# Optimization experiments

Hardware: AMD Instinct MI355X
Metric: run time of the kernel (lower is better)

## Reference

```python
import jax, jax.numpy as jnp
import numpy as np

B, L, Q, C, D = 256, 200, 20000, 500, 256
S = L - 1  # 199 recurrent steps, bounded by time_embed (200) / state banks (199)


def setup_inputs() -> dict:
    key = jax.random.key(0)
    ks = iter(jax.random.split(key, 48))
    nk = lambda: next(ks)

    def lin(fi, fo):
        w = jax.random.normal(nk(), (fo, fi), jnp.float32) * 0.02
        b = jnp.zeros((fo,), jnp.float32)
        return w, b

    inp = {}
    inp["question_seq"] = jax.random.randint(nk(), (B, L), 0, Q, dtype=jnp.int32)
    inp["concept_seq"] = jax.random.randint(nk(), (B, L), 0, C, dtype=jnp.int32)
    inp["correctness_seq"] = jax.random.randint(nk(), (B, L), 0, 2, dtype=jnp.int32)
    # parameters (torch.rand -> uniform[0,1))
    inp["pro_embed"] = jax.random.uniform(nk(), (Q, D), jnp.float32)
    inp["skill_embed"] = jax.random.uniform(nk(), (C, D), jnp.float32)
    inp["ans_embed"] = jax.random.uniform(nk(), (2, D), jnp.float32)
    inp["time_embed"] = jax.random.uniform(nk(), (200, D), jnp.float32)
    inp["ls_state"] = jax.random.uniform(nk(), (1, D), jnp.float32)
    inp["pro_state0"] = jax.random.uniform(nk(), (S, D), jnp.float32)
    inp["skill_state0"] = jax.random.uniform(nk(), (S, D), jnp.float32)
    inp["akt_pro_diff"] = jax.random.uniform(nk(), (Q, 1), jnp.float32)
    inp["akt_pro_change"] = jax.random.uniform(nk(), (C, D), jnp.float32)
    inp["Wpf"], inp["bpf"] = lin(2 * D, D)
    inp["Wps"], inp["bps"] = lin(2 * D, D)
    inp["Wsf"], inp["bsf"] = lin(2 * D, D)
    inp["Wss"], inp["bss"] = lin(2 * D, D)
    inp["Waf"], inp["baf"] = lin(2 * D, D)
    inp["Was"], inp["bas"] = lin(2 * D, D)
    inp["Wo1"], inp["bo1"] = lin(4 * D, D)
    inp["Wo2"], inp["bo2"] = lin(D, 1)
    return inp


def reference(question_seq, concept_seq, correctness_seq, pro_embed, skill_embed,
              ans_embed, time_embed, ls_state, pro_state0, skill_state0,
              akt_pro_diff, akt_pro_change, Wpf, bpf, Wps, bps, Wsf, bsf,
              Wss, bss, Waf, baf, Was, bas, Wo1, bo1, Wo2, bo2):
    nq = question_seq[:, 1:]   # [B,S] next problem ids
    nc = concept_seq[:, 1:]    # [B,S] next skill ids
    na = correctness_seq[:, 1:]
    # fused question embedding (Rasch-style): q + c + diff(q)*change(c)
    npe = pro_embed[nq] + skill_embed[nc] + akt_pro_diff[nq] * akt_pro_change[nc]  # [B,S,D]
    nx = npe + ans_embed[na]   # interaction embedding
    atge = time_embed[1]       # all_time_gap == 1 for every (b,t)
    bidx = jnp.arange(B)

    def step(carry, xs):
        lpt, lct, ps, ss, ast = carry  # last-time tables, time-indexed state banks, global state
        t, pe, x, ip, ic = xs
        lp_t = lpt[bidx, ip]           # [B] last time this problem was seen
        lp_s = ps[bidx, lp_t]          # [B,D] gather from problem state bank
        lc_t = lct[bidx, ic]
        lc_s = ss[bidx, lc_t]
        tge = time_embed[t - lp_t]
        ctge = time_embed[t - lc_t]
        # forget gates (dropout p=0 -> identity)
        lp_s = lp_s * jax.nn.sigmoid(jnp.concatenate([lp_s, tge], -1) @ Wpf.T + bpf)
        lc_s = lc_s * jax.nn.sigmoid(jnp.concatenate([lc_s, ctge], -1) @ Wsf.T + bsf)
        la_s = ast * jax.nn.sigmoid(
            jnp.concatenate([ast, jnp.broadcast_to(atge, ast.shape)], -1) @ Waf.T + baf)
        final = jnp.concatenate([la_s, lp_s, lc_s, pe], -1)  # [B,4D]
        P = jax.nn.sigmoid(jax.nn.relu(final @ Wo1.T + bo1) @ Wo2.T + bo2)[:, 0]
        # state updates
        a_new = la_s + jnp.tanh(jnp.concatenate([la_s, x], -1) @ Was.T + bas)
        p_new = lp_s + jnp.tanh(jnp.concatenate([lp_s, x], -1) @ Wps.T + bps)
        c_new = lc_s + jnp.tanh(jnp.concatenate([lc_s, x], -1) @ Wss.T + bss)
        lpt = lpt.at[bidx, ip].set(t)
        lct = lct.at[bidx, ic].set(t)
        ps = ps.at[:, t].set(p_new)   # scatter into time slot t
        ss = ss.at[:, t].set(c_new)
        return (lpt, lct, ps, ss, a_new), P

    init = (jnp.zeros((B, Q), jnp.int32),
            jnp.zeros((B, C), jnp.int32),
            jnp.broadcast_to(pro_state0[None], (B, S, D)) + 0.0,
            jnp.broadcast_to(skill_state0[None], (B, S, D)) + 0.0,
            jnp.broadcast_to(ls_state, (B, D)) + 0.0)
    ts = jnp.arange(S, dtype=jnp.int32)
    xs = (ts, jnp.swapaxes(npe, 0, 1), jnp.swapaxes(nx, 0, 1), nq.T, nc.T)
    _, Ps = jax.lax.scan(step, init, xs)  # Ps: [S,B]
    return Ps.T  # [B,S]
```

## Files before the change

kernel.cpp:

```cpp
#include <hip/hip_runtime.h>
#include <cstdint>
#include <cstddef>

#define B_ 256
#define L_ 200
#define S_ 199
#define D_ 256
#define Q_ 20000
#define C_ 500

#define OFF_TEPF 0u
#define OFF_TESF 204800u
#define OFF_CAF  409600u
#define OFF_PPF  410624u
#define OFF_PSF  541696u
#define OFF_PAF  672768u
#define OFF_PAS  803840u
#define OFF_PPS  1065984u
#define OFF_PSS  1328128u
#define OFF_PO1  1590272u
#define OFF_PS   2114560u
#define OFF_SS   54281216u

__device__ __forceinline__ unsigned bf16_rne(float f) {
  unsigned u = __float_as_uint(f);
  return (u + 0x7fffu + ((u >> 16) & 1u)) >> 16;
}

__global__ void te_kernel(const float* __restrict__ te,
                          const float* __restrict__ Wpf, const float* __restrict__ bpf,
                          const float* __restrict__ Wsf, const float* __restrict__ bsf,
                          float* __restrict__ TEpf, float* __restrict__ TEsf) {
  int idx = blockIdx.x * 256 + threadIdx.x;
  int tau = idx >> 8, d = idx & 255;
  const float* ter = te + (tau << 8);
  const float* wp = Wpf + d * 512 + 256;
  const float* ws = Wsf + d * 512 + 256;
  float ap = 0.f, as = 0.f;
  for (int k = 0; k < 256; ++k) {
    float x = ter[k];
    ap = fmaf(x, wp[k], ap);
    as = fmaf(x, ws[k], as);
  }
  TEpf[idx] = ap + bpf[d];
  TEsf[idx] = as + bsf[d];
}

__global__ void caf_kernel(const float* __restrict__ te, const float* __restrict__ Waf,
                           const float* __restrict__ baf, float* __restrict__ CAF) {
  int d = threadIdx.x;
  const float* ter = te + 256;
  const float* wa = Waf + d * 512 + 256;
  float a = 0.f;
  for (int k = 0; k < 256; ++k) a = fmaf(ter[k], wa[k], a);
  CAF[d] = a + baf[d];
}

__global__ void pack_kernel(const float* __restrict__ W, uint2* __restrict__ out, int fi) {
  int k4 = blockIdx.x, d = threadIdx.x;
  const float* r = W + d * fi + (k4 << 2);
  unsigned p0 = bf16_rne(r[0]) | (bf16_rne(r[1]) << 16);
  unsigned p1 = bf16_rne(r[2]) | (bf16_rne(r[3]) << 16);
  out[k4 * 256 + d] = make_uint2(p0, p1);
}

__device__ __forceinline__ float upfma(uint2 w, float4 x, float acc) {
  acc = fmaf(__uint_as_float(w.x << 16), x.x, acc);
  acc = fmaf(__uint_as_float(w.x & 0xffff0000u), x.y, acc);
  acc = fmaf(__uint_as_float(w.y << 16), x.z, acc);
  acc = fmaf(__uint_as_float(w.y & 0xffff0000u), x.w, acc);
  return acc;
}

__device__ __forceinline__ float sigf(float z) { return 1.f / (1.f + __expf(-z)); }
__device__ __forceinline__ float tanh_fast(float z) { return 1.f - 2.f / (__expf(2.f * z) + 1.f); }

__global__ __launch_bounds__(256)
void scan_kernel(const int* __restrict__ q_seq, const int* __restrict__ c_seq,
                 const int* __restrict__ a_seq,
                 const float* __restrict__ pro_embed, const float* __restrict__ skill_embed,
                 const float* __restrict__ ans_embed,
                 const float* __restrict__ ls_state,
                 const float* __restrict__ pro_state0, const float* __restrict__ skill_state0,
                 const float* __restrict__ akt_diff, const float* __restrict__ akt_change,
                 const float* __restrict__ TEpf, const float* __restrict__ TEsf,
                 const float* __restrict__ CAF,
                 const uint2* __restrict__ Ppf, const uint2* __restrict__ Psf,
                 const uint2* __restrict__ Paf,
                 const uint2* __restrict__ Pas, const uint2* __restrict__ Pps,
                 const uint2* __restrict__ Pss, const uint2* __restrict__ Po1,
                 const float* __restrict__ bas, const float* __restrict__ bps,
                 const float* __restrict__ bss, const float* __restrict__ bo1,
                 const float* __restrict__ Wo2, const float* __restrict__ bo2,
                 float* __restrict__ ps, float* __restrict__ ss,
                 float* __restrict__ out) {
  const int b = blockIdx.x;
  const int d = threadIdx.x;

  __shared__ float s_ast[256], s_lp[256], s_lc[256], s_tge[256], s_ctge[256];
  __shared__ float s_pe[256], s_x[256], s_la[256], s_lp2[256], s_lc2[256];
  __shared__ float s_caf[256], s_wo2[256], s_bas[256], s_bps[256], s_bss[256], s_bo1[256];
  __shared__ int s_lqt[Q_];
  __shared__ int s_lct[C_];
  __shared__ float s_red[4];

  s_ast[d] = ls_state[d];
  s_caf[d] = CAF[d];
  s_wo2[d] = Wo2[d];
  s_bas[d] = bas[d]; s_bps[d] = bps[d]; s_bss[d] = bss[d]; s_bo1[d] = bo1[d];
  s_lct[d] = 0;
  if (d + 256 < C_) s_lct[d + 256] = 0;
#pragma clang loop unroll(disable)
  for (int i = d; i < Q_; i += 256) s_lqt[i] = 0;

  float* psb = ps + (size_t)b * S_ * D_;
  float* ssb = ss + (size_t)b * S_ * D_;
  psb[d] = pro_state0[d];
  ssb[d] = skill_state0[d];
  const int* qs = q_seq + b * L_;
  const int* cs = c_seq + b * L_;
  const int* as_ = a_seq + b * L_;
  const float bo2v = bo2[0];
  __syncthreads();

#pragma clang loop unroll(disable)
  for (int t = 0; t < S_; ++t) {
    const int ip = qs[t + 1];
    const int ic = cs[t + 1];
    const int ia = as_[t + 1];
    const int lp_t = s_lqt[ip];
    const int lc_t = s_lct[ic];

    s_lp[d]  = psb[lp_t * D_ + d];
    s_lc[d]  = ssb[lc_t * D_ + d];
    s_tge[d] = TEpf[(t - lp_t) * D_ + d];
    s_ctge[d]= TEsf[(t - lc_t) * D_ + d];
    float pe = pro_embed[ip * D_ + d] + skill_embed[ic * D_ + d]
             + akt_diff[ip] * akt_change[ic * D_ + d];
    s_pe[d] = pe;
    s_x[d]  = pe + ans_embed[ia * D_ + d];
    __syncthreads();

    float a0 = 0.f, a1 = 0.f, a2 = 0.f;
    {
      const float4* xp = (const float4*)s_lp;
      const float4* xs = (const float4*)s_lc;
      const float4* xa = (const float4*)s_ast;
#pragma unroll 4
      for (int k = 0; k < 64; ++k) {
        a0 = upfma(Ppf[k * 256 + d], xp[k], a0);
        a1 = upfma(Psf[k * 256 + d], xs[k], a1);
        a2 = upfma(Paf[k * 256 + d], xa[k], a2);
      }
    }
    const float lp2 = s_lp[d]  * sigf(a0 + s_tge[d]);
    const float lc2 = s_lc[d]  * sigf(a1 + s_ctge[d]);
    const float la2 = s_ast[d] * sigf(a2 + s_caf[d]);
    s_la[d] = la2; s_lp2[d] = lp2; s_lc2[d] = lc2;
    if (d == 0) { s_lqt[ip] = t; s_lct[ic] = t; }
    __syncthreads();

    float accO = 0.f, accA = 0.f, accP = 0.f, accC = 0.f;
    {
      const float4* xla = (const float4*)s_la;
      const float4* xlp = (const float4*)s_lp2;
      const float4* xlc = (const float4*)s_lc2;
      const float4* xpe = (const float4*)s_pe;
      const float4* xx  = (const float4*)s_x;
#pragma unroll 4
      for (int k = 0; k < 64; ++k) {
        float4 v = xla[k];
        accO = upfma(Po1[k * 256 + d], v, accO);
        accA = upfma(Pas[k * 256 + d], v, accA);
      }
#pragma unroll 4
      for (int k = 0; k < 64; ++k) {
        float4 v = xlp[k];
        accO = upfma(Po1[(64 + k) * 256 + d], v, accO);
        accP = upfma(Pps[k * 256 + d], v, accP);
      }
#pragma unroll 4
      for (int k = 0; k < 64; ++k) {
        float4 v = xlc[k];
        accO = upfma(Po1[(128 + k) * 256 + d], v, accO);
        accC = upfma(Pss[k * 256 + d], v, accC);
      }
#pragma unroll 4
      for (int k = 0; k < 64; ++k) {
        float4 v = xpe[k];
        accO = upfma(Po1[(192 + k) * 256 + d], v, accO);
      }
#pragma unroll 4
      for (int k = 0; k < 64; ++k) {
        float4 v = xx[k];
        accA = upfma(Pas[(64 + k) * 256 + d], v, accA);
        accP = upfma(Pps[(64 + k) * 256 + d], v, accP);
        accC = upfma(Pss[(64 + k) * 256 + d], v, accC);
      }
    }

    const float o1 = fmaxf(accO + s_bo1[d], 0.f);
    float r = o1 * s_wo2[d];
#pragma unroll
    for (int off = 32; off; off >>= 1) r += __shfl_down(r, off);

    const float a_new = la2 + tanh_fast(accA + s_bas[d]);
    const float p_new = lp2 + tanh_fast(accP + s_bps[d]);
    const float c_new = lc2 + tanh_fast(accC + s_bss[d]);
    psb[t * D_ + d] = p_new;
    ssb[t * D_ + d] = c_new;
    s_ast[d] = a_new;
    if ((d & 63) == 0) s_red[d >> 6] = r;
    __syncthreads();
    if (d == 0) {
      float z = s_red[0] + s_red[1] + s_red[2] + s_red[3] + bo2v;
      out[b * S_ + t] = 1.f / (1.f + __expf(-z));
    }
  }
}

extern "C" void kernel_launch(void* const* d_in, const int* in_sizes, int n_in,
                              void* d_out, int out_size, void* d_ws, size_t ws_size,
                              hipStream_t stream) {
  const int*   q_seq        = (const int*)d_in[0];
  const int*   c_seq        = (const int*)d_in[1];
  const int*   a_seq        = (const int*)d_in[2];
  const float* pro_embed    = (const float*)d_in[3];
  const float* skill_embed  = (const float*)d_in[4];
  const float* ans_embed    = (const float*)d_in[5];
  const float* time_embed   = (const float*)d_in[6];
  const float* ls_state     = (const float*)d_in[7];
  const float* pro_state0   = (const float*)d_in[8];
  const float* skill_state0 = (const float*)d_in[9];
  const float* akt_diff     = (const float*)d_in[10];
  const float* akt_change   = (const float*)d_in[11];
  const float* Wpf = (const float*)d_in[12]; const float* bpf = (const float*)d_in[13];
  const float* Wps = (const float*)d_in[14]; const float* bps = (const float*)d_in[15];
  const float* Wsf = (const float*)d_in[16]; const float* bsf = (const float*)d_in[17];
  const float* Wss = (const float*)d_in[18]; const float* bss = (const float*)d_in[19];
  const float* Waf = (const float*)d_in[20]; const float* baf = (const float*)d_in[21];
  const float* Was = (const float*)d_in[22]; const float* bas = (const float*)d_in[23];
  const float* Wo1 = (const float*)d_in[24]; const float* bo1 = (const float*)d_in[25];
  const float* Wo2 = (const float*)d_in[26]; const float* bo2 = (const float*)d_in[27];

  char* ws = (char*)d_ws;
  float* TEpf = (float*)(ws + OFF_TEPF);
  float* TEsf = (float*)(ws + OFF_TESF);
  float* CAF  = (float*)(ws + OFF_CAF);
  uint2* Ppf  = (uint2*)(ws + OFF_PPF);
  uint2* Psf  = (uint2*)(ws + OFF_PSF);
  uint2* Paf  = (uint2*)(ws + OFF_PAF);
  uint2* Pas  = (uint2*)(ws + OFF_PAS);
  uint2* Pps  = (uint2*)(ws + OFF_PPS);
  uint2* Pss  = (uint2*)(ws + OFF_PSS);
  uint2* Po1  = (uint2*)(ws + OFF_PO1);
  float* ps   = (float*)(ws + OFF_PS);
  float* ssb  = (float*)(ws + OFF_SS);
  float* out  = (float*)d_out;

  te_kernel<<<200, 256, 0, stream>>>(time_embed, Wpf, bpf, Wsf, bsf, TEpf, TEsf);
  caf_kernel<<<1, 256, 0, stream>>>(time_embed, Waf, baf, CAF);

  pack_kernel<<<64, 256, 0, stream>>>(Wpf, Ppf, 512);
  pack_kernel<<<64, 256, 0, stream>>>(Wsf, Psf, 512);
  pack_kernel<<<64, 256, 0, stream>>>(Waf, Paf, 512);
  pack_kernel<<<128, 256, 0, stream>>>(Was, Pas, 512);
  pack_kernel<<<128, 256, 0, stream>>>(Wps, Pps, 512);
  pack_kernel<<<128, 256, 0, stream>>>(Wss, Pss, 512);
  pack_kernel<<<256, 256, 0, stream>>>(Wo1, Po1, 1024);

  scan_kernel<<<B_, 256, 0, stream>>>(q_seq, c_seq, a_seq,
                                      pro_embed, skill_embed, ans_embed,
                                      ls_state, pro_state0, skill_state0,
                                      akt_diff, akt_change,
                                      TEpf, TEsf, CAF,
                                      Ppf, Psf, Paf, Pas, Pps, Pss, Po1,
                                      bas, bps, bss, bo1, Wo2, bo2,
                                      ps, ssb, out);
}
```

Baseline: 6.034 ms.

## Split reduction dimension across 4x threads and use fp16 packed dot products

The scan kernel now runs 1024 threads per block, with four thread groups each handling a quarter of the K dimension of every matvec. Partial sums are combined through shared memory. The kernel also switches weights and activations from bf16/fp32 to fp16 and uses the fdot2 instruction on 8-element packed loads. This is meant to shorten the serial per-step latency of the recurrent loop, at the cost of extra syncs, shared-memory reductions and reduced fp16 precision.

```diff
diff --git a/kernel.cpp b/kernel.cpp
--- a/kernel.cpp
+++ b/kernel.cpp
@@ -1,4 +1,5 @@
 #include <hip/hip_runtime.h>
+#include <hip/hip_fp16.h>
 #include <cstdint>
 #include <cstddef>
 
@@ -21,11 +22,6 @@
 #define OFF_PO1  1590272u
 #define OFF_PS   2114560u
 #define OFF_SS   54281216u
-
-__device__ __forceinline__ unsigned bf16_rne(float f) {
-  unsigned u = __float_as_uint(f);
-  return (u + 0x7fffu + ((u >> 16) & 1u)) >> 16;
-}
 
 __global__ void te_kernel(const float* __restrict__ te,
                           const float* __restrict__ Wpf, const float* __restrict__ bpf,
@@ -56,26 +52,45 @@
   CAF[d] = a + baf[d];
 }
 
-__global__ void pack_kernel(const float* __restrict__ W, uint2* __restrict__ out, int fi) {
-  int k4 = blockIdx.x, d = threadIdx.x;
-  const float* r = W + d * fi + (k4 << 2);
-  unsigned p0 = bf16_rne(r[0]) | (bf16_rne(r[1]) << 16);
-  unsigned p1 = bf16_rne(r[2]) | (bf16_rne(r[3]) << 16);
-  out[k4 * 256 + d] = make_uint2(p0, p1);
-}
-
-__device__ __forceinline__ float upfma(uint2 w, float4 x, float acc) {
-  acc = fmaf(__uint_as_float(w.x << 16), x.x, acc);
-  acc = fmaf(__uint_as_float(w.x & 0xffff0000u), x.y, acc);
-  acc = fmaf(__uint_as_float(w.y << 16), x.z, acc);
-  acc = fmaf(__uint_as_float(w.y & 0xffff0000u), x.w, acc);
+__device__ __forceinline__ unsigned pk2(float a, float b) {
+  __half2 h = __floats2half2_rn(a, b);
+  return *(unsigned*)&h;
+}
+
+__global__ void pack_kernel(const float* __restrict__ W, uint4* __restrict__ out, int fi) {
+  int k8 = blockIdx.x, d = threadIdx.x;
+  const float* r = W + d * fi + (k8 << 3);
+  out[k8 * 256 + d] = make_uint4(pk2(r[0], r[1]), pk2(r[2], r[3]),
+                                 pk2(r[4], r[5]), pk2(r[6], r[7]));
+}
+
+typedef _Float16 h2v __attribute__((ext_vector_type(2)));
+union U2H { unsigned u; h2v h; __half2 hh; };
+
+__device__ __forceinline__ float fd2(unsigned w, unsigned x, float acc) {
+#if __has_builtin(__builtin_amdgcn_fdot2)
+  U2H a; a.u = w; U2H b; b.u = x;
+  return __builtin_amdgcn_fdot2(a.h, b.h, acc, false);
+#else
+  U2H a; a.u = w; U2H b; b.u = x;
+  acc = fmaf(__low2float(a.hh),  __low2float(b.hh),  acc);
+  acc = fmaf(__high2float(a.hh), __high2float(b.hh), acc);
+  return acc;
+#endif
+}
+
+__device__ __forceinline__ float dot8(uint4 w, uint4 x, float acc) {
+  acc = fd2(w.x, x.x, acc);
+  acc = fd2(w.y, x.y, acc);
+  acc = fd2(w.z, x.z, acc);
+  acc = fd2(w.w, x.w, acc);
   return acc;
 }
 
 __device__ __forceinline__ float sigf(float z) { return 1.f / (1.f + __expf(-z)); }
 __device__ __forceinline__ float tanh_fast(float z) { return 1.f - 2.f / (__expf(2.f * z) + 1.f); }
 
-__global__ __launch_bounds__(256)
+__global__ __launch_bounds__(1024)
 void scan_kernel(const int* __restrict__ q_seq, const int* __restrict__ c_seq,
                  const int* __restrict__ a_seq,
                  const float* __restrict__ pro_embed, const float* __restrict__ skill_embed,
@@ -85,38 +100,45 @@
                  const float* __restrict__ akt_diff, const float* __restrict__ akt_change,
                  const float* __restrict__ TEpf, const float* __restrict__ TEsf,
                  const float* __restrict__ CAF,
-                 const uint2* __restrict__ Ppf, const uint2* __restrict__ Psf,
-                 const uint2* __restrict__ Paf,
-                 const uint2* __restrict__ Pas, const uint2* __restrict__ Pps,
-                 const uint2* __restrict__ Pss, const uint2* __restrict__ Po1,
+                 const uint4* __restrict__ Ppf, const uint4* __restrict__ Psf,
+                 const uint4* __restrict__ Paf,
+                 const uint4* __restrict__ Pas, const uint4* __restrict__ Pps,
+                 const uint4* __restrict__ Pss, const uint4* __restrict__ Po1,
                  const float* __restrict__ bas, const float* __restrict__ bps,
                  const float* __restrict__ bss, const float* __restrict__ bo1,
                  const float* __restrict__ Wo2, const float* __restrict__ bo2,
                  float* __restrict__ ps, float* __restrict__ ss,
                  float* __restrict__ out) {
   const int b = blockIdx.x;
-  const int d = threadIdx.x;
-
-  __shared__ float s_ast[256], s_lp[256], s_lc[256], s_tge[256], s_ctge[256];
-  __shared__ float s_pe[256], s_x[256], s_la[256], s_lp2[256], s_lc2[256];
-  __shared__ float s_caf[256], s_wo2[256], s_bas[256], s_bps[256], s_bss[256], s_bo1[256];
+  const int tid = threadIdx.x;
+  const int d = tid & 255;
+  const int h = tid >> 8;
+
   __shared__ int s_lqt[Q_];
   __shared__ int s_lct[C_];
+  __shared__ float s_lp_f[256], s_lc_f[256], s_ast_f[256];
+  __shared__ float s_la_f[256], s_lp2_f[256], s_lc2_f[256];
+  __shared__ float s_tge[256], s_ctge[256];
+  __shared__ float s_caf[256], s_wo2[256], s_bo1[256], s_bas[256], s_bps[256], s_bss[256];
+  __shared__ __align__(16) __half s_lp_h[256], s_lc_h[256], s_ast_h[256];
+  __shared__ __align__(16) __half s_la_h[256], s_lp2_h[256], s_lc2_h[256];
+  __shared__ __align__(16) __half s_pe_h[256], s_x_h[256];
+  __shared__ float s_pa[1024], s_pb[1024], s_pc[1024], s_pd[1024];
   __shared__ float s_red[4];
 
-  s_ast[d] = ls_state[d];
-  s_caf[d] = CAF[d];
-  s_wo2[d] = Wo2[d];
-  s_bas[d] = bas[d]; s_bps[d] = bps[d]; s_bss[d] = bss[d]; s_bo1[d] = bo1[d];
-  s_lct[d] = 0;
-  if (d + 256 < C_) s_lct[d + 256] = 0;
-#pragma clang loop unroll(disable)
-  for (int i = d; i < Q_; i += 256) s_lqt[i] = 0;
+  for (int i = tid; i < Q_; i += 1024) s_lqt[i] = 0;
+  if (tid < C_) s_lct[tid] = 0;
 
   float* psb = ps + (size_t)b * S_ * D_;
   float* ssb = ss + (size_t)b * S_ * D_;
-  psb[d] = pro_state0[d];
-  ssb[d] = skill_state0[d];
+  if (h == 0) {
+    float a = ls_state[d];
+    s_ast_f[d] = a; s_ast_h[d] = __float2half(a);
+    psb[d] = pro_state0[d];
+    ssb[d] = skill_state0[d];
+    s_caf[d] = CAF[d]; s_wo2[d] = Wo2[d];
+    s_bo1[d] = bo1[d]; s_bas[d] = bas[d]; s_bps[d] = bps[d]; s_bss[d] = bss[d];
+  }
   const int* qs = q_seq + b * L_;
   const int* cs = c_seq + b * L_;
   const int* as_ = a_seq + b * L_;
@@ -131,88 +153,106 @@
     const int lp_t = s_lqt[ip];
     const int lc_t = s_lct[ic];
 
-    s_lp[d]  = psb[lp_t * D_ + d];
-    s_lc[d]  = ssb[lc_t * D_ + d];
-    s_tge[d] = TEpf[(t - lp_t) * D_ + d];
-    s_ctge[d]= TEsf[(t - lc_t) * D_ + d];
-    float pe = pro_embed[ip * D_ + d] + skill_embed[ic * D_ + d]
-             + akt_diff[ip] * akt_change[ic * D_ + d];
-    s_pe[d] = pe;
-    s_x[d]  = pe + ans_embed[ia * D_ + d];
-    __syncthreads();
-
-    float a0 = 0.f, a1 = 0.f, a2 = 0.f;
+    if (h == 0) {
+      float lp = psb[lp_t * D_ + d];
+      s_lp_f[d] = lp; s_lp_h[d] = __float2half(lp);
+    } else if (h == 1) {
+      float lc = ssb[lc_t * D_ + d];
+      s_lc_f[d] = lc; s_lc_h[d] = __float2half(lc);
+    } else if (h == 2) {
+      s_tge[d] = TEpf[(t - lp_t) * D_ + d];
+      float pe = pro_embed[ip * D_ + d] + skill_embed[ic * D_ + d]
+               + akt_diff[ip] * akt_change[ic * D_ + d];
+      s_pe_h[d] = __float2half(pe);
+    } else {
+      s_ctge[d] = TEsf[(t - lc_t) * D_ + d];
+      float pe = pro_embed[ip * D_ + d] + skill_embed[ic * D_ + d]
+               + akt_diff[ip] * akt_change[ic * D_ + d];
+      s_x_h[d] = __float2half(pe + ans_embed[ia * D_ + d]);
+    }
+    __syncthreads();
+
     {
-      const float4* xp = (const float4*)s_lp;
-      const float4* xs = (const float4*)s_lc;
-      const float4* xa = (const float4*)s_ast;
+      const uint4* xlp = (const uint4*)s_lp_h;
+      const uint4* xlc = (const uint4*)s_lc_h;
+      const uint4* xas = (const uint4*)s_ast_h;
+      const int j0 = h << 3;
+      float a0 = 0.f, a1 = 0.f, a2 = 0.f;
+#pragma unroll 8
+      for (int kk = 0; kk < 8; ++kk) { int j = j0 + kk; a0 = dot8(Ppf[j * 256 + d], xlp[j], a0); }
+#pragma unroll 8
+      for (int kk = 0; kk < 8; ++kk) { int j = j0 + kk; a1 = dot8(Psf[j * 256 + d], xlc[j], a1); }
+#pragma unroll 8
+      for (int kk = 0; kk < 8; ++kk) { int j = j0 + kk; a2 = dot8(Paf[j * 256 + d], xas[j], a2); }
+      s_pa[tid] = a0; s_pb[tid] = a1; s_pc[tid] = a2;
+    }
+    __syncthreads();
+
+    if (h == 0) {
+      float g0 = s_pa[d] + s_pa[d + 256] + s_pa[d + 512] + s_pa[d + 768];
+      float g1 = s_pb[d] + s_pb[d + 256] + s_pb[d + 512] + s_pb[d + 768];
+      float g2 = s_pc[d] + s_pc[d + 256] + s_pc[d + 512] + s_pc[d + 768];
+      float lp2 = s_lp_f[d]  * sigf(g0 + s_tge[d]);
+      float lc2 = s_lc_f[d]  * sigf(g1 + s_ctge[d]);
+      float la2 = s_ast_f[d] * sigf(g2 + s_caf[d]);
+      s_lp2_f[d] = lp2; s_lp2_h[d] = __float2half(lp2);
+      s_lc2_f[d] = lc2; s_lc2_h[d] = __float2half(lc2);
+      s_la_f[d]  = la2; s_la_h[d]  = __float2half(la2);
+      if (d == 0) { s_lqt[ip] = t; s_lct[ic] = t; }
+    }
+    __syncthreads();
+
+    {
+      const uint4* xla = (const uint4*)s_la_h;
+      const uint4* xlp = (const uint4*)s_lp2_h;
+      const uint4* xlc = (const uint4*)s_lc2_h;
+      const uint4* xpe = (const uint4*)s_pe_h;
+      const uint4* xx  = (const uint4*)s_x_h;
+      const int j0 = h << 3;
+      float accO = 0.f, accA = 0.f, accP = 0.f, accC = 0.f;
 #pragma unroll 4
-      for (int k = 0; k < 64; ++k) {
-        a0 = upfma(Ppf[k * 256 + d], xp[k], a0);
-        a1 = upfma(Psf[k * 256 + d], xs[k], a1);
-        a2 = upfma(Paf[k * 256 + d], xa[k], a2);
-      }
-    }
-    const float lp2 = s_lp[d]  * sigf(a0 + s_tge[d]);
-    const float lc2 = s_lc[d]  * sigf(a1 + s_ctge[d]);
-    const float la2 = s_ast[d] * sigf(a2 + s_caf[d]);
-    s_la[d] = la2; s_lp2[d] = lp2; s_lc2[d] = lc2;
-    if (d == 0) { s_lqt[ip] = t; s_lct[ic] = t; }
-    __syncthreads();
-
-    float accO = 0.f, accA = 0.f, accP = 0.f, accC = 0.f;
-    {
-      const float4* xla = (const float4*)s_la;
-      const float4* xlp = (const float4*)s_lp2;
-      const float4* xlc = (const float4*)s_lc2;
-      const float4* xpe = (const float4*)s_pe;
-      const float4* xx  = (const float4*)s_x;
+      for (int kk = 0; kk < 8; ++kk) { int j = j0 + kk; uint4 v = xla[j];
+        accO = dot8(Po1[j * 256 + d], v, accO);
+        accA = dot8(Pas[j * 256 + d], v, accA); }
 #pragma unroll 4
-      for (int k = 0; k < 64; ++k) {
-        float4 v = xla[k];
-        accO = upfma(Po1[k * 256 + d], v, accO);
-        accA = upfma(Pas[k * 256 + d], v, accA);
-      }
+      for (int kk = 0; kk < 8; ++kk) { int j = j0 + kk; uint4 v = xlp[j];
+        accO = dot8(Po1[(32 + j) * 256 + d], v, accO);
+        accP = dot8(Pps[j * 256 + d], v, accP); }
 #pragma unroll 4
-      for (int k = 0; k < 64; ++k) {
-        float4 v = xlp[k];
-        accO = upfma(Po1[(64 + k) * 256 + d], v, accO);
-        accP = upfma(Pps[k * 256 + d], v, accP);
-      }
+      for (int kk = 0; kk < 8; ++kk) { int j = j0 + kk; uint4 v = xlc[j];
+        accO = dot8(Po1[(64 + j) * 256 + d], v, accO);
+        accC = dot8(Pss[j * 256 + d], v, accC); }
+#pragma unroll 8
+      for (int kk = 0; kk < 8; ++kk) { int j = j0 + kk;
+        accO = dot8(Po1[(96 + j) * 256 + d], xpe[j], accO); }
 #pragma unroll 4
-      for (int k = 0; k < 64; ++k) {
-        float4 v = xlc[k];
-        accO = upfma(Po1[(128 + k) * 256 + d], v, accO);
-        accC = upfma(Pss[k * 256 + d], v, accC);
-      }
-#pragma unroll 4
-      for (int k = 0; k < 64; ++k) {
-        float4 v = xpe[k];
-        accO = upfma(Po1[(192 + k) * 256 + d], v, accO);
-      }
-#pragma unroll 4
-      for (int k = 0; k < 64; ++k) {
-        float4 v = xx[k];
-        accA = upfma(Pas[(64 + k) * 256 + d], v, accA);
-        accP = upfma(Pps[(64 + k) * 256 + d], v, accP);
-        accC = upfma(Pss[(64 + k) * 256 + d], v, accC);
-      }
-    }
-
-    const float o1 = fmaxf(accO + s_bo1[d], 0.f);
-    float r = o1 * s_wo2[d];
+      for (int kk = 0; kk < 8; ++kk) { int j = j0 + kk; uint4 v = xx[j];
+        accA = dot8(Pas[(32 + j) * 256 + d], v, accA);
+        accP = dot8(Pps[(32 + j) * 256 + d], v, accP);
+        accC = dot8(Pss[(32 + j) * 256 + d], v, accC); }
+      s_pa[tid] = accO; s_pb[tid] = accA; s_pc[tid] = accP; s_pd[tid] = accC;
+    }
+    __syncthreads();
+
+    if (h == 0) {
+      float accO = s_pa[d] + s_pa[d + 256] + s_pa[d + 512] + s_pa[d + 768];
+      float accA = s_pb[d] + s_pb[d + 256] + s_pb[d + 512] + s_pb[d + 768];
+      float accP = s_pc[d] + s_pc[d + 256] + s_pc[d + 512] + s_pc[d + 768];
+      float accC = s_pd[d] + s_pd[d + 256] + s_pd[d + 512] + s_pd[d + 768];
+      float o1 = fmaxf(accO + s_bo1[d], 0.f);
+      float r = o1 * s_wo2[d];
 #pragma unroll
-    for (int off = 32; off; off >>= 1) r += __shfl_down(r, off);
-
-    const float a_new = la2 + tanh_fast(accA + s_bas[d]);
-    const float p_new = lp2 + tanh_fast(accP + s_bps[d]);
-    const float c_new = lc2 + tanh_fast(accC + s_bss[d]);
-    psb[t * D_ + d] = p_new;
-    ssb[t * D_ + d] = c_new;
-    s_ast[d] = a_new;
-    if ((d & 63) == 0) s_red[d >> 6] = r;
-    __syncthreads();
-    if (d == 0) {
+      for (int off = 32; off; off >>= 1) r += __shfl_down(r, off);
+      float a_new = s_la_f[d]  + tanh_fast(accA + s_bas[d]);
+      float p_new = s_lp2_f[d] + tanh_fast(accP + s_bps[d]);
+      float c_new = s_lc2_f[d] + tanh_fast(accC + s_bss[d]);
+      s_ast_f[d] = a_new; s_ast_h[d] = __float2half(a_new);
+      psb[t * D_ + d] = p_new;
+      ssb[t * D_ + d] = c_new;
+      if ((d & 63) == 0) s_red[d >> 6] = r;
+    }
+    __syncthreads();
+    if (tid == 0) {
       float z = s_red[0] + s_red[1] + s_red[2] + s_red[3] + bo2v;
       out[b * S_ + t] = 1.f / (1.f + __expf(-z));
     }
@@ -247,13 +287,13 @@
   float* TEpf = (float*)(ws + OFF_TEPF);
   float* TEsf = (float*)(ws + OFF_TESF);
   float* CAF  = (float*)(ws + OFF_CAF);
-  uint2* Ppf  = (uint2*)(ws + OFF_PPF);
-  uint2* Psf  = (uint2*)(ws + OFF_PSF);
-  uint2* Paf  = (uint2*)(ws + OFF_PAF);
-  uint2* Pas  = (uint2*)(ws + OFF_PAS);
-  uint2* Pps  = (uint2*)(ws + OFF_PPS);
-  uint2* Pss  = (uint2*)(ws + OFF_PSS);
-  uint2* Po1  = (uint2*)(ws + OFF_PO1);
+  uint4* Ppf  = (uint4*)(ws + OFF_PPF);
+  uint4* Psf  = (uint4*)(ws + OFF_PSF);
+  uint4* Paf  = (uint4*)(ws + OFF_PAF);
+  uint4* Pas  = (uint4*)(ws + OFF_PAS);
+  uint4* Pps  = (uint4*)(ws + OFF_PPS);
+  uint4* Pss  = (uint4*)(ws + OFF_PSS);
+  uint4* Po1  = (uint4*)(ws + OFF_PO1);
   float* ps   = (float*)(ws + OFF_PS);
   float* ssb  = (float*)(ws + OFF_SS);
   float* out  = (float*)d_out;
@@ -261,20 +301,20 @@
   te_kernel<<<200, 256, 0, stream>>>(time_embed, Wpf, bpf, Wsf, bsf, TEpf, TEsf);
   caf_kernel<<<1, 256, 0, stream>>>(time_embed, Waf, baf, CAF);
 
-  pack_kernel<<<64, 256, 0, stream>>>(Wpf, Ppf, 512);
-  pack_kernel<<<64, 256, 0, stream>>>(Wsf, Psf, 512);
-  pack_kernel<<<64, 256, 0, stream>>>(Waf, Paf, 512);
-  pack_kernel<<<128, 256, 0, stream>>>(Was, Pas, 512);
-  pack_kernel<<<128, 256, 0, stream>>>(Wps, Pps, 512);
-  pack_kernel<<<128, 256, 0, stream>>>(Wss, Pss, 512);
-  pack_kernel<<<256, 256, 0, stream>>>(Wo1, Po1, 1024);
-
-  scan_kernel<<<B_, 256, 0, stream>>>(q_seq, c_seq, a_seq,
-                                      pro_embed, skill_embed, ans_embed,
-                                      ls_state, pro_state0, skill_state0,
-                                      akt_diff, akt_change,
-                                      TEpf, TEsf, CAF,
-                                      Ppf, Psf, Paf, Pas, Pps, Pss, Po1,
-                                      bas, bps, bss, bo1, Wo2, bo2,
-                                      ps, ssb, out);
-}
+  pack_kernel<<<32, 256, 0, stream>>>(Wpf, Ppf, 512);
+  pack_kernel<<<32, 256, 0, stream>>>(Wsf, Psf, 512);
+  pack_kernel<<<32, 256, 0, stream>>>(Waf, Paf, 512);
+  pack_kernel<<<64, 256, 0, stream>>>(Was, Pas, 512);
+  pack_kernel<<<64, 256, 0, stream>>>(Wps, Pps, 512);
+  pack_kernel<<<64, 256, 0, stream>>>(Wss, Pss, 512);
+  pack_kernel<<<128, 256, 0, stream>>>(Wo1, Po1, 1024);
+
+  scan_kernel<<<B_, 1024, 0, stream>>>(q_seq, c_seq, a_seq,
+                                       pro_embed, skill_embed, ans_embed,
+                                       ls_state, pro_state0, skill_state0,
+                                       akt_diff, akt_change,
+                                       TEpf, TEsf, CAF,
+                                       Ppf, Psf, Paf, Pas, Pps, Pss, Po1,
+                                       bas, bps, bss, bo1, Wo2, bo2,
+                                       ps, ssb, out);
+}
```

New measurement: 9.056 ms. 50.1% more time.
